# Kernel tuning notes

Measured on AMD Instinct MI355X. Metric: run time of the kernel, lower is better.

Reference implementation:

```python
import jax, jax.numpy as jnp
import numpy as np

B, N, D_IN, D_OUT = 16, 2048, 64, 64


def setup_inputs() -> dict:
    key = jax.random.key(0)
    k1, k2, k3, k4, k5 = jax.random.split(key, 5)
    x = jax.random.normal(k1, (B, N, D_IN), dtype=jnp.float32)
    weight = jax.random.normal(k2, (D_IN, D_OUT), dtype=jnp.float32) * (1.0 / np.sqrt(D_OUT))
    att = jax.random.uniform(k3, (N, N), dtype=jnp.float32, minval=-1.0 / np.sqrt(D_OUT), maxval=1.0 / np.sqrt(D_OUT))
    bias = jax.random.normal(k4, (D_OUT,), dtype=jnp.float32) * (1.0 / np.sqrt(D_OUT))
    mask = jax.random.randint(k5, (N, N), 0, 2, dtype=jnp.int32)
    return {"x": x, "weight": weight, "att": att, "bias": bias, "mask": mask}


def reference(x, weight, att, bias, mask):
    # x: [B, N, D_in]; weight: [D_in, D_out]; att, mask: [N, N]; bias: [D_out]
    support = jnp.einsum('bnd,de->bne', x, weight)          # [B, N, D_out]
    mup = jnp.einsum('bnd,bmd->bnm', x, x)                  # [B, N, N]
    norms = jnp.linalg.norm(x, axis=-1, keepdims=True)      # [B, N, 1]
    mdown = norms * jnp.swapaxes(norms, 1, 2)               # [B, N, N] outer product of norms
    w = mup / mdown                                         # cosine similarity
    adjacent = (att * mask.astype(jnp.float32)) * w         # masked attention * cosine weights
    out = jnp.einsum('bnm,bme->bne', adjacent, support)     # [B, N, D_out]
    return out + bias
```

## Files before the change

### kernel.cpp

```cpp
#include <hip/hip_runtime.h>
#include <stdint.h>

#define NN 2048

typedef short bf8_t __attribute__((ext_vector_type(8)));
typedef float f32x4 __attribute__((ext_vector_type(4)));

__device__ __forceinline__ unsigned int rbf(float f) {
    unsigned int u = __builtin_bit_cast(unsigned int, f);
    return u + 0x7FFFu + ((u >> 16) & 1u);
}
__device__ __forceinline__ unsigned short f2b(float f) { return (unsigned short)(rbf(f) >> 16); }
__device__ __forceinline__ unsigned int pk2(float lo, float hi) {
    return (rbf(lo) >> 16) | (rbf(hi) & 0xFFFF0000u);
}
__device__ __forceinline__ unsigned int pk2t(float lo, float hi) {
    unsigned int ulo = __builtin_bit_cast(unsigned int, lo) + 0x8000u;
    unsigned int uhi = __builtin_bit_cast(unsigned int, hi) + 0x8000u;
    return (ulo >> 16) | (uhi & 0xFFFF0000u);
}

__global__ __launch_bounds__(256) void prep_kernel(
    const float* __restrict__ x, const float* __restrict__ w,
    const float* __restrict__ att, const int* __restrict__ mask,
    unsigned short* __restrict__ xB, unsigned short* __restrict__ sB,
    unsigned short* __restrict__ amB)
{
    __shared__ unsigned short lds[4 * 64 * 72];
    __shared__ float part[64][4];

    const int t = threadIdx.x;
    const int row = t >> 2, seg = t & 3;
    const int wv = t >> 6, l = t & 63, c = l & 15, q = l >> 4;

    if (blockIdx.x < 512) {
        unsigned short* xs = lds;
        unsigned short* xt = lds + 4608;
        unsigned short* Wt = lds + 9216;
        unsigned short* st = lds + 13824;
        const int j = blockIdx.x;
        const int nt = (j & 7) * 4 + ((j >> 3) & 3);
        const int b = j >> 5;

        float4 xq[4], wq[4];
        const float* xp = x + ((size_t)(b * NN + nt * 64 + row)) * 64 + seg * 16;
        const float* wp = w + row * 64 + seg * 16;
        #pragma unroll
        for (int i = 0; i < 4; ++i) { xq[i] = ((const float4*)xp)[i]; wq[i] = ((const float4*)wp)[i]; }
        float ss = 0.f;
        #pragma unroll
        for (int i = 0; i < 4; ++i)
            ss += xq[i].x * xq[i].x + xq[i].y * xq[i].y + xq[i].z * xq[i].z + xq[i].w * xq[i].w;
        part[row][seg] = ss;
        #pragma unroll
        for (int i = 0; i < 4; ++i) {
            ((unsigned int*)&xs[row * 72 + seg * 16])[i * 2]     = pk2(xq[i].x, xq[i].y);
            ((unsigned int*)&xs[row * 72 + seg * 16])[i * 2 + 1] = pk2(xq[i].z, xq[i].w);
            Wt[(seg * 16 + i * 4 + 0) * 72 + row] = f2b(wq[i].x);
            Wt[(seg * 16 + i * 4 + 1) * 72 + row] = f2b(wq[i].y);
            Wt[(seg * 16 + i * 4 + 2) * 72 + row] = f2b(wq[i].z);
            Wt[(seg * 16 + i * 4 + 3) * 72 + row] = f2b(wq[i].w);
        }
        __syncthreads();

        const float rinv = 1.0f / sqrtf(part[row][0] + part[row][1] + part[row][2] + part[row][3]);
        #pragma unroll
        for (int i = 0; i < 4; ++i) {
            ((unsigned int*)&xt[row * 72 + seg * 16])[i * 2]     = pk2(xq[i].x * rinv, xq[i].y * rinv);
            ((unsigned int*)&xt[row * 72 + seg * 16])[i * 2 + 1] = pk2(xq[i].z * rinv, xq[i].w * rinv);
        }
        __syncthreads();

        {
            bf8_t h0 = *(const bf8_t*)&xt[(wv * 16 + c) * 72 + q * 8];
            bf8_t h1 = *(const bf8_t*)&xt[(wv * 16 + c) * 72 + 32 + q * 8];
            unsigned short* base = xB + ((size_t)(b * 32 + nt)) * 4096 + wv * 1024 + l * 8;
            *(bf8_t*)base = h0;
            *(bf8_t*)(base + 512) = h1;
        }
        {
            bf8_t a0 = *(const bf8_t*)&xs[(wv * 16 + c) * 72 + q * 8];
            bf8_t a1 = *(const bf8_t*)&xs[(wv * 16 + c) * 72 + 32 + q * 8];
            #pragma unroll
            for (int cb = 0; cb < 4; ++cb) {
                bf8_t b0 = *(const bf8_t*)&Wt[(cb * 16 + c) * 72 + q * 8];
                bf8_t b1 = *(const bf8_t*)&Wt[(cb * 16 + c) * 72 + 32 + q * 8];
                f32x4 z = (f32x4){0.f, 0.f, 0.f, 0.f};
                z = __builtin_amdgcn_mfma_f32_16x16x32_bf16(a0, b0, z, 0, 0, 0);
                z = __builtin_amdgcn_mfma_f32_16x16x32_bf16(a1, b1, z, 0, 0, 0);
                #pragma unroll
                for (int r = 0; r < 4; ++r)
                    st[(cb * 16 + c) * 72 + wv * 16 + q * 4 + r] = f2b(z[r]);
            }
        }
        __syncthreads();
        {
            bf8_t h0 = *(const bf8_t*)&st[(wv * 16 + c) * 72 + q * 8];
            bf8_t h1 = *(const bf8_t*)&st[(wv * 16 + c) * 72 + 32 + q * 8];
            unsigned short* base = sB + ((size_t)(b * 32 + nt)) * 4096 + wv * 1024 + l * 8;
            *(bf8_t*)base = h0;
            *(bf8_t*)(base + 512) = h1;
        }
    } else {
        unsigned short* amt = lds;
        const int bid2 = blockIdx.x - 512;
        const int it = (bid2 & 7) * 4 + ((bid2 >> 3) & 3);
        const int mc = bid2 >> 5;
        const size_t g = ((size_t)(it * 64 + row)) * NN + mc * 64 + seg * 16;
        #pragma unroll
        for (int i = 0; i < 4; ++i) {
            float4 a = *(const float4*)(att + g + i * 4);
            int4   m = *(const int4*)(mask + g + i * 4);
            ((unsigned int*)&amt[row * 72 + seg * 16])[i * 2] =
                pk2(a.x * (float)m.x, a.y * (float)m.y);
            ((unsigned int*)&amt[row * 72 + seg * 16])[i * 2 + 1] =
                pk2(a.z * (float)m.z, a.w * (float)m.w);
        }
        __syncthreads();
        unsigned int ww[8];
        #pragma unroll
        for (int rbi = 0; rbi < 4; ++rbi) {
            #pragma unroll
            for (int rp = 0; rp < 2; ++rp) {
                unsigned int lo = amt[(rbi * 16 + c) * 72 + wv * 16 + q * 4 + rp * 2];
                unsigned int hi = amt[(rbi * 16 + c) * 72 + wv * 16 + q * 4 + rp * 2 + 1];
                ww[rbi * 2 + rp] = lo | (hi << 16);
            }
        }
        unsigned short* base = amB + ((size_t)(it * 32 + mc)) * 4096 + wv * 1024 + l * 8;
        *(uint4*)base         = *(uint4*)&ww[0];
        *(uint4*)(base + 512) = *(uint4*)&ww[4];
    }
}

__global__ __launch_bounds__(256, 2) void gcn_kernel(
    const unsigned short* __restrict__ xB, const unsigned short* __restrict__ sB,
    const unsigned short* __restrict__ amB, const float* __restrict__ bias,
    float* __restrict__ out)
{
    __shared__ unsigned short Adj[4][64 * 72];
    const int t = threadIdx.x;
    const int wm = t >> 6, l = t & 63, c = l & 15, q = l >> 4;
    const int bid = blockIdx.x;
    const int r8 = bid & 31, b = bid >> 5;
    const int it = (r8 & 7) * 4 + (r8 >> 3);

    const unsigned short* xit = xB + ((size_t)(b * 32 + it)) * 4096;
    bf8_t xi0[4], xi1[4];
    #pragma unroll
    for (int rb = 0; rb < 4; ++rb) {
        xi0[rb] = *(const bf8_t*)(xit + rb * 1024 + l * 8);
        xi1[rb] = *(const bf8_t*)(xit + rb * 1024 + 512 + l * 8);
    }
    f32x4 acc[4][4];
    #pragma unroll
    for (int rb = 0; rb < 4; ++rb)
        #pragma unroll
        for (int cb = 0; cb < 4; ++cb) acc[rb][cb] = (f32x4){0.f, 0.f, 0.f, 0.f};

    unsigned short* adj = &Adj[wm][0];

    bf8_t xmA0[4], xmA1[4], xmB0[4], xmB1[4];
    uint4 amA[8], amBv[8];
    {
        const unsigned short* xmt = xB + ((size_t)(b * 32 + wm)) * 4096;
        const unsigned short* amp = amB + ((size_t)(it * 32 + wm)) * 4096;
        #pragma unroll
        for (int cb = 0; cb < 4; ++cb) {
            xmA0[cb] = *(const bf8_t*)(xmt + cb * 1024 + l * 8);
            xmA1[cb] = *(const bf8_t*)(xmt + cb * 1024 + 512 + l * 8);
        }
        #pragma unroll
        for (int j = 0; j < 8; ++j) amA[j] = *(const uint4*)(amp + j * 512 + l * 8);
    }

    #pragma unroll
    for (int tt = 0; tt < 8; ++tt) {
        const int mc = wm + tt * 4;

        if (tt < 7) {
            const unsigned short* xmn = xB + ((size_t)(b * 32 + mc + 4)) * 4096;
            const unsigned short* amn = amB + ((size_t)(it * 32 + mc + 4)) * 4096;
            if ((tt & 1) == 0) {
                #pragma unroll
                for (int cb = 0; cb < 4; ++cb) {
                    xmB0[cb] = *(const bf8_t*)(xmn + cb * 1024 + l * 8);
                    xmB1[cb] = *(const bf8_t*)(xmn + cb * 1024 + 512 + l * 8);
                }
                #pragma unroll
                for (int j = 0; j < 8; ++j) amBv[j] = *(const uint4*)(amn + j * 512 + l * 8);
            } else {
                #pragma unroll
                for (int cb = 0; cb < 4; ++cb) {
                    xmA0[cb] = *(const bf8_t*)(xmn + cb * 1024 + l * 8);
                    xmA1[cb] = *(const bf8_t*)(xmn + cb * 1024 + 512 + l * 8);
                }
                #pragma unroll
                for (int j = 0; j < 8; ++j) amA[j] = *(const uint4*)(amn + j * 512 + l * 8);
            }
        }
        const unsigned short* smt = sB + ((size_t)(b * 32 + mc)) * 4096;
        bf8_t sm0[4], sm1[4];
        #pragma unroll
        for (int cb = 0; cb < 4; ++cb) {
            sm0[cb] = *(const bf8_t*)(smt + cb * 1024 + l * 8);
            sm1[cb] = *(const bf8_t*)(smt + cb * 1024 + 512 + l * 8);
        }

        const bf8_t* xm0 = (tt & 1) ? xmB0 : xmA0;
        const bf8_t* xm1 = (tt & 1) ? xmB1 : xmA1;
        const uint4* amv = (tt & 1) ? amBv : amA;

        #pragma unroll
        for (int cbm = 0; cbm < 4; ++cbm) {
            #pragma unroll
            for (int rbi = 0; rbi < 4; ++rbi) {
                f32x4 z = (f32x4){0.f, 0.f, 0.f, 0.f};
                z = __builtin_amdgcn_mfma_f32_16x16x32_bf16(xm0[cbm], xi0[rbi], z, 0, 0, 0);
                z = __builtin_amdgcn_mfma_f32_16x16x32_bf16(xm1[cbm], xi1[rbi], z, 0, 0, 0);
                const unsigned int w0 = ((const unsigned int*)&amv[cbm * 2 + (rbi >> 1)])[(rbi & 1) * 2 + 0];
                const unsigned int w1 = ((const unsigned int*)&amv[cbm * 2 + (rbi >> 1)])[(rbi & 1) * 2 + 1];
                const float a0f = __builtin_bit_cast(float, w0 << 16);
                const float a1f = __builtin_bit_cast(float, w0 & 0xFFFF0000u);
                const float a2f = __builtin_bit_cast(float, w1 << 16);
                const float a3f = __builtin_bit_cast(float, w1 & 0xFFFF0000u);
                uint2 p;
                p.x = pk2t(z[0] * a0f, z[1] * a1f);
                p.y = pk2t(z[2] * a2f, z[3] * a3f);
                *(uint2*)&adj[(rbi * 16 + c) * 72 + cbm * 16 + q * 4] = p;
            }
        }
        #pragma unroll
        for (int rb = 0; rb < 4; ++rb) {
            bf8_t p0 = *(const bf8_t*)&adj[(rb * 16 + c) * 72 + q * 8];
            bf8_t p1 = *(const bf8_t*)&adj[(rb * 16 + c) * 72 + 32 + q * 8];
            #pragma unroll
            for (int cb = 0; cb < 4; ++cb) {
                acc[rb][cb] = __builtin_amdgcn_mfma_f32_16x16x32_bf16(p0, sm0[cb], acc[rb][cb], 0, 0, 0);
                acc[rb][cb] = __builtin_amdgcn_mfma_f32_16x16x32_bf16(p1, sm1[cb], acc[rb][cb], 0, 0, 0);
            }
        }
    }

    float* red = (float*)&Adj[0][0];
    const int i0 = it * 64;
    for (int h = 0; h < 2; ++h) {
        __syncthreads();
        #pragma unroll
        for (int rb2 = 0; rb2 < 2; ++rb2) {
            const int rb = h * 2 + rb2;
            #pragma unroll
            for (int cb = 0; cb < 4; ++cb)
                #pragma unroll
                for (int r = 0; r < 4; ++r)
                    red[wm * 2176 + (rb2 * 16 + q * 4 + r) * 68 + cb * 16 + c] = acc[rb][cb][r];
        }
        __syncthreads();
        #pragma unroll
        for (int rnd = 0; rnd < 8; ++rnd) {
            const int idx = rnd * 256 + t;
            const int row = idx >> 6, col = idx & 63;
            const float s = red[0 * 2176 + row * 68 + col] + red[1 * 2176 + row * 68 + col]
                          + red[2 * 2176 + row * 68 + col] + red[3 * 2176 + row * 68 + col];
            out[((size_t)(b * NN + i0 + h * 32 + row)) * 64 + col] = s + bias[col];
        }
    }
}

extern "C" void kernel_launch(void* const* d_in, const int* in_sizes, int n_in,
                              void* d_out, int out_size, void* d_ws, size_t ws_size,
                              hipStream_t stream) {
    const float* x    = (const float*)d_in[0];
    const float* w    = (const float*)d_in[1];
    const float* att  = (const float*)d_in[2];
    const float* bias = (const float*)d_in[3];
    const int*   mask = (const int*)d_in[4];
    float* out = (float*)d_out;

    unsigned short* xB  = (unsigned short*)d_ws;
    unsigned short* sB  = xB + (size_t)2 * 1024 * 1024;
    unsigned short* amB = sB + (size_t)2 * 1024 * 1024;

    prep_kernel<<<dim3(1536), dim3(256), 0, stream>>>(x, w, att, mask, xB, sB, amB);
    gcn_kernel<<<dim3(512), dim3(256), 0, stream>>>(xB, sB, amB, bias, out);
}
```

Before: 117.6 us.

## Fuse prep and GCN kernels with a grid-wide atomic barrier

Merges the preprocessing kernel and the main GCN kernel into one persistent launch of 512 blocks. Each block converts two att*mask tiles plus its own x/support tile, then waits on a global atomic counter barrier before the main loop. The block's own normalized x tile is read back from LDS instead of global memory. This removes a kernel launch and the gap between kernels, but adds a memset, a spin barrier that assumes all 512 blocks are co-resident, and less parallelism in the prep phase.

```diff
diff --git a/kernel.cpp b/kernel.cpp
--- a/kernel.cpp
+++ b/kernel.cpp
@@ -20,11 +20,13 @@
     return (ulo >> 16) | (uhi & 0xFFFF0000u);
 }
 
-__global__ __launch_bounds__(256) void prep_kernel(
+__global__ __launch_bounds__(256, 2) void fused_kernel(
     const float* __restrict__ x, const float* __restrict__ w,
     const float* __restrict__ att, const int* __restrict__ mask,
+    const float* __restrict__ bias,
     unsigned short* __restrict__ xB, unsigned short* __restrict__ sB,
-    unsigned short* __restrict__ amB)
+    unsigned short* __restrict__ amB, unsigned int* __restrict__ ctr,
+    float* __restrict__ out)
 {
     __shared__ unsigned short lds[4 * 64 * 72];
     __shared__ float part[64][4];
@@ -32,18 +34,53 @@
     const int t = threadIdx.x;
     const int row = t >> 2, seg = t & 3;
     const int wv = t >> 6, l = t & 63, c = l & 15, q = l >> 4;
-
-    if (blockIdx.x < 512) {
+    const int bid = blockIdx.x;
+    const int r8 = bid & 31, b = bid >> 5;
+    const int it = (r8 & 7) * 4 + (r8 >> 3);
+
+    {
+        const int xcd = bid & 7, k = bid >> 3;
+        const int itp = xcd * 4 + (k & 3);
+        unsigned short* amt = lds;
+        #pragma unroll 1
+        for (int rep = 0; rep < 2; ++rep) {
+            const int mcp = (k >> 2) + rep * 16;
+            const size_t g = ((size_t)(itp * 64 + row)) * NN + mcp * 64 + seg * 16;
+            #pragma unroll
+            for (int i = 0; i < 4; ++i) {
+                float4 a = *(const float4*)(att + g + i * 4);
+                int4   m = *(const int4*)(mask + g + i * 4);
+                ((unsigned int*)&amt[row * 72 + seg * 16])[i * 2] =
+                    pk2(a.x * (float)m.x, a.y * (float)m.y);
+                ((unsigned int*)&amt[row * 72 + seg * 16])[i * 2 + 1] =
+                    pk2(a.z * (float)m.z, a.w * (float)m.w);
+            }
+            __syncthreads();
+            unsigned int ww[8];
+            #pragma unroll
+            for (int rbi = 0; rbi < 4; ++rbi) {
+                #pragma unroll
+                for (int rp = 0; rp < 2; ++rp) {
+                    unsigned int lo = amt[(rbi * 16 + c) * 72 + wv * 16 + q * 4 + rp * 2];
+                    unsigned int hi = amt[(rbi * 16 + c) * 72 + wv * 16 + q * 4 + rp * 2 + 1];
+                    ww[rbi * 2 + rp] = lo | (hi << 16);
+                }
+            }
+            unsigned short* base = amB + ((size_t)(itp * 32 + mcp)) * 4096 + wv * 1024 + l * 8;
+            *(uint4*)base         = *(uint4*)&ww[0];
+            *(uint4*)(base + 512) = *(uint4*)&ww[4];
+            __syncthreads();
+        }
+    }
+
+    {
         unsigned short* xs = lds;
         unsigned short* xt = lds + 4608;
         unsigned short* Wt = lds + 9216;
         unsigned short* st = lds + 13824;
-        const int j = blockIdx.x;
-        const int nt = (j & 7) * 4 + ((j >> 3) & 3);
-        const int b = j >> 5;
 
         float4 xq[4], wq[4];
-        const float* xp = x + ((size_t)(b * NN + nt * 64 + row)) * 64 + seg * 16;
+        const float* xp = x + ((size_t)(b * NN + it * 64 + row)) * 64 + seg * 16;
         const float* wp = w + row * 64 + seg * 16;
         #pragma unroll
         for (int i = 0; i < 4; ++i) { xq[i] = ((const float4*)xp)[i]; wq[i] = ((const float4*)wp)[i]; }
@@ -74,7 +111,7 @@
         {
             bf8_t h0 = *(const bf8_t*)&xt[(wv * 16 + c) * 72 + q * 8];
             bf8_t h1 = *(const bf8_t*)&xt[(wv * 16 + c) * 72 + 32 + q * 8];
-            unsigned short* base = xB + ((size_t)(b * 32 + nt)) * 4096 + wv * 1024 + l * 8;
+            unsigned short* base = xB + ((size_t)(b * 32 + it)) * 4096 + wv * 1024 + l * 8;
             *(bf8_t*)base = h0;
             *(bf8_t*)(base + 512) = h1;
         }
@@ -97,68 +134,38 @@
         {
             bf8_t h0 = *(const bf8_t*)&st[(wv * 16 + c) * 72 + q * 8];
             bf8_t h1 = *(const bf8_t*)&st[(wv * 16 + c) * 72 + 32 + q * 8];
-            unsigned short* base = sB + ((size_t)(b * 32 + nt)) * 4096 + wv * 1024 + l * 8;
+            unsigned short* base = sB + ((size_t)(b * 32 + it)) * 4096 + wv * 1024 + l * 8;
             *(bf8_t*)base = h0;
             *(bf8_t*)(base + 512) = h1;
         }
-    } else {
-        unsigned short* amt = lds;
-        const int bid2 = blockIdx.x - 512;
-        const int it = (bid2 & 7) * 4 + ((bid2 >> 3) & 3);
-        const int mc = bid2 >> 5;
-        const size_t g = ((size_t)(it * 64 + row)) * NN + mc * 64 + seg * 16;
-        #pragma unroll
-        for (int i = 0; i < 4; ++i) {
-            float4 a = *(const float4*)(att + g + i * 4);
-            int4   m = *(const int4*)(mask + g + i * 4);
-            ((unsigned int*)&amt[row * 72 + seg * 16])[i * 2] =
-                pk2(a.x * (float)m.x, a.y * (float)m.y);
-            ((unsigned int*)&amt[row * 72 + seg * 16])[i * 2 + 1] =
-                pk2(a.z * (float)m.z, a.w * (float)m.w);
-        }
-        __syncthreads();
-        unsigned int ww[8];
-        #pragma unroll
-        for (int rbi = 0; rbi < 4; ++rbi) {
-            #pragma unroll
-            for (int rp = 0; rp < 2; ++rp) {
-                unsigned int lo = amt[(rbi * 16 + c) * 72 + wv * 16 + q * 4 + rp * 2];
-                unsigned int hi = amt[(rbi * 16 + c) * 72 + wv * 16 + q * 4 + rp * 2 + 1];
-                ww[rbi * 2 + rp] = lo | (hi << 16);
-            }
-        }
-        unsigned short* base = amB + ((size_t)(it * 32 + mc)) * 4096 + wv * 1024 + l * 8;
-        *(uint4*)base         = *(uint4*)&ww[0];
-        *(uint4*)(base + 512) = *(uint4*)&ww[4];
-    }
-}
-
-__global__ __launch_bounds__(256, 2) void gcn_kernel(
-    const unsigned short* __restrict__ xB, const unsigned short* __restrict__ sB,
-    const unsigned short* __restrict__ amB, const float* __restrict__ bias,
-    float* __restrict__ out)
-{
-    __shared__ unsigned short Adj[4][64 * 72];
-    const int t = threadIdx.x;
-    const int wm = t >> 6, l = t & 63, c = l & 15, q = l >> 4;
-    const int bid = blockIdx.x;
-    const int r8 = bid & 31, b = bid >> 5;
-    const int it = (r8 & 7) * 4 + (r8 >> 3);
-
-    const unsigned short* xit = xB + ((size_t)(b * 32 + it)) * 4096;
+    }
+
+    __threadfence();
+    __syncthreads();
+    if (t == 0) {
+        atomicAdd(ctr, 1u);
+        while (__hip_atomic_load(ctr, __ATOMIC_ACQUIRE, __HIP_MEMORY_SCOPE_AGENT) < 512u)
+            __builtin_amdgcn_s_sleep(2);
+    }
+    __syncthreads();
+    __threadfence();
+
     bf8_t xi0[4], xi1[4];
     #pragma unroll
     for (int rb = 0; rb < 4; ++rb) {
-        xi0[rb] = *(const bf8_t*)(xit + rb * 1024 + l * 8);
-        xi1[rb] = *(const bf8_t*)(xit + rb * 1024 + 512 + l * 8);
-    }
+        xi0[rb] = *(const bf8_t*)&lds[4608 + (rb * 16 + c) * 72 + q * 8];
+        xi1[rb] = *(const bf8_t*)&lds[4608 + (rb * 16 + c) * 72 + 32 + q * 8];
+    }
+    __syncthreads();
+
     f32x4 acc[4][4];
     #pragma unroll
     for (int rb = 0; rb < 4; ++rb)
         #pragma unroll
         for (int cb = 0; cb < 4; ++cb) acc[rb][cb] = (f32x4){0.f, 0.f, 0.f, 0.f};
 
-    unsigned short* adj = &Adj[wm][0];
+    unsigned short* adj = &lds[wv * 4608];
+    const int wm = wv;
 
     bf8_t xmA0[4], xmA1[4], xmB0[4], xmB1[4];
     uint4 amA[8], amBv[8];
@@ -242,7 +249,7 @@
         }
     }
 
-    float* red = (float*)&Adj[0][0];
+    float* red = (float*)&lds[0];
     const int i0 = it * 64;
     for (int h = 0; h < 2; ++h) {
         __syncthreads();
@@ -259,10 +266,10 @@
         #pragma unroll
         for (int rnd = 0; rnd < 8; ++rnd) {
             const int idx = rnd * 256 + t;
-            const int row = idx >> 6, col = idx & 63;
-            const float s = red[0 * 2176 + row * 68 + col] + red[1 * 2176 + row * 68 + col]
-                          + red[2 * 2176 + row * 68 + col] + red[3 * 2176 + row * 68 + col];
-            out[((size_t)(b * NN + i0 + h * 32 + row)) * 64 + col] = s + bias[col];
+            const int rw = idx >> 6, col = idx & 63;
+            const float s = red[0 * 2176 + rw * 68 + col] + red[1 * 2176 + rw * 68 + col]
+                          + red[2 * 2176 + rw * 68 + col] + red[3 * 2176 + rw * 68 + col];
+            out[((size_t)(b * NN + i0 + h * 32 + rw)) * 64 + col] = s + bias[col];
         }
     }
 }
@@ -280,7 +287,9 @@
     unsigned short* xB  = (unsigned short*)d_ws;
     unsigned short* sB  = xB + (size_t)2 * 1024 * 1024;
     unsigned short* amB = sB + (size_t)2 * 1024 * 1024;
-
-    prep_kernel<<<dim3(1536), dim3(256), 0, stream>>>(x, w, att, mask, xB, sB, amB);
-    gcn_kernel<<<dim3(512), dim3(256), 0, stream>>>(xB, sB, amB, bias, out);
-}
+    unsigned int*  ctr  = (unsigned int*)((char*)d_ws + ((size_t)16 << 20));
+
+    hipMemsetAsync(ctr, 0, 64, stream);
+    fused_kernel<<<dim3(512), dim3(256), 0, stream>>>(
+        x, w, att, mask, bias, xB, sB, amB, ctr, out);
+}
```

After: 234.6 us. +99.5%, slower.
